# Performance work log

Measured on AMD Instinct MI355X. Metric: run time of the kernel, lower is better.

The kernel has to match this reference:

```python
import jax, jax.numpy as jnp
import numpy as np
from jax import lax

N = 512  # neurons (== input features in this base class)

@jax.custom_vjp
def spike_fn(x):
    # Heaviside spike with fast-sigmoid surrogate gradient (standard for LIF SNNs)
    return (x > 0.0).astype(x.dtype)

def _spike_fwd(x):
    return spike_fn(x), x

def _spike_bwd(x, g):
    sg = 1.0 / (1.0 + 10.0 * jnp.abs(x)) ** 2
    return (g * sg,)

spike_fn.defvjp(_spike_fwd, _spike_bwd)

def setup_inputs() -> dict:
    key = jax.random.key(0)
    k1, k2, k3, k4, k5, k6 = jax.random.split(key, 6)
    B, T = 64, 1000
    scale = 1.0 / np.sqrt(N)
    return {
        "input_batch": jax.random.normal(k1, (B, T, N), dtype=jnp.float32),
        "state_snn": jnp.zeros((2, B, N), dtype=jnp.float32),  # [v; s]
        "state_LI": jnp.zeros((B, N), dtype=jnp.float32),
        "W1": jax.random.normal(k2, (N, N), dtype=jnp.float32) * scale,
        "W2": jax.random.normal(k3, (N, N), dtype=jnp.float32) * scale,
        "leak_v": jax.random.uniform(k4, (N,), dtype=jnp.float32, minval=0.8, maxval=0.99),
        "leak_i": jax.random.uniform(k5, (N,), dtype=jnp.float32, minval=0.8, maxval=0.99),
        "thresh": jax.random.uniform(k6, (N,), dtype=jnp.float32, minval=0.5, maxval=1.5),
    }

def reference(input_batch, state_snn, state_LI, W1, W2, leak_v, leak_i, thresh):
    # input_batch: [B, T, N]; time loop expressed as lax.scan over T
    v0, s0 = state_snn[0], state_snn[1]
    xs = jnp.swapaxes(input_batch, 0, 1)  # [T, B, N]

    def step(carry, x_t):
        v, s, u = carry
        ff = x_t @ W1.T                        # LIF feed-forward current
        v = leak_v * v * (1.0 - s) + ff        # leak + reset-to-zero on spike
        s = spike_fn(v - thresh)               # spike generation
        u = leak_i * u + s @ W2.T              # leaky-integrator readout
        return (v, s, u), (s, jnp.stack([v, s]), u)

    _, (spikes, states_snn, decoded) = lax.scan(step, (v0, s0, state_LI), xs)
    # spikes: [T,B,N], states_snn: [T,2,B,N], decoded: [T,B,N]
    return spikes, states_snn, decoded
```

## Files before the change

kernel.cpp:

```cpp
#include <hip/hip_runtime.h>

#define T_STEPS 1000
#define B_SZ 64
#define N_SZ 512
#define BN_TOT (B_SZ * N_SZ)
#define TBN   ((size_t)T_STEPS * BN_TOT)

typedef __attribute__((ext_vector_type(4))) float f32x4;
typedef __attribute__((ext_vector_type(8))) short bf16x8;
typedef unsigned short ushort_t;

__global__ __launch_bounds__(256, 2)
void sgemm_abt(const float* __restrict__ A, const float* __restrict__ W,
               float* __restrict__ C)
{
    constexpr int K = 512;
    constexpr int BK = 32;
    constexpr int LDT = 128 + 4;
    __shared__ float As[BK][LDT];
    __shared__ float Bs[BK][LDT];

    const int tid = threadIdx.x;
    const int tx = tid & 15;
    const int ty = tid >> 4;
    const size_t m0 = (size_t)blockIdx.y * 128;
    const int n0 = blockIdx.x * 128;

    float acc[8][8];
#pragma unroll
    for (int i = 0; i < 8; ++i)
#pragma unroll
        for (int j = 0; j < 8; ++j) acc[i][j] = 0.0f;

    for (int k0 = 0; k0 < K; k0 += BK) {
#pragma unroll
        for (int p = 0; p < 4; ++p) {
            int i = tid + p * 256;
            int r = i >> 3;
            int q = i & 7;
            float4 va = *(const float4*)(A + (m0 + r) * K + k0 + q * 4);
            As[q * 4 + 0][r] = va.x; As[q * 4 + 1][r] = va.y;
            As[q * 4 + 2][r] = va.z; As[q * 4 + 3][r] = va.w;
            float4 vb = *(const float4*)(W + (size_t)(n0 + r) * K + k0 + q * 4);
            Bs[q * 4 + 0][r] = vb.x; Bs[q * 4 + 1][r] = vb.y;
            Bs[q * 4 + 2][r] = vb.z; Bs[q * 4 + 3][r] = vb.w;
        }
        __syncthreads();
#pragma unroll
        for (int k = 0; k < BK; ++k) {
            float a[8], b[8];
            *(float4*)&a[0] = *(const float4*)&As[k][ty * 8];
            *(float4*)&a[4] = *(const float4*)&As[k][ty * 8 + 4];
            *(float4*)&b[0] = *(const float4*)&Bs[k][tx * 4];
            *(float4*)&b[4] = *(const float4*)&Bs[k][tx * 4 + 64];
#pragma unroll
            for (int i = 0; i < 8; ++i)
#pragma unroll
                for (int j = 0; j < 8; ++j)
                    acc[i][j] = fmaf(a[i], b[j], acc[i][j]);
        }
        __syncthreads();
    }

#pragma unroll
    for (int i = 0; i < 8; ++i) {
        float* cp = C + (m0 + ty * 8 + i) * 512 + n0 + tx * 4;
        *(float4*)cp        = make_float4(acc[i][0], acc[i][1], acc[i][2], acc[i][3]);
        *(float4*)(cp + 64) = make_float4(acc[i][4], acc[i][5], acc[i][6], acc[i][7]);
    }
}

__global__ __launch_bounds__(256)
void w2_split(const float* __restrict__ W2, ushort_t* __restrict__ Wc)
{
    int i = blockIdx.x * 256 + threadIdx.x;
    int n = i >> 9, k = i & 511;
    float w = W2[i];
    unsigned wb = __float_as_uint(w);
    float h = __uint_as_float(wb & 0xFFFF0000u);
    float r1 = w - h;
    unsigned r1b = __float_as_uint(r1);
    size_t base = (size_t)n * 1024 + k;
    Wc[base]       = (ushort_t)(wb >> 16);
    Wc[base + 512] = (ushort_t)(r1b >> 16);
}

__global__ __launch_bounds__(256, 2)
void gemm2_mfma(const ushort_t* __restrict__ S, const ushort_t* __restrict__ Wc,
                float* __restrict__ C)
{
    constexpr int NT = 1024 / 32;
    __shared__ ushort_t As[2][128 * 32];
    __shared__ ushort_t Bs[2][128 * 32];

    const int tid = threadIdx.x;
    const int m0 = blockIdx.y * 128;
    const int n0 = blockIdx.x * 128;
    const int wid = tid >> 6;
    const int lane = tid & 63;
    const int wm = (wid >> 1) * 64;
    const int wn = (wid & 1) * 64;
    const int fr = lane & 15;
    const int fq = lane >> 4;

    f32x4 acc[4][4] = {};

    const int rA = tid >> 2;
    const int cA = (tid & 3) * 8;

#define STAGE(buf, t)                                                        \
    {                                                                        \
        const int k0_ = (t) * 32;                                            \
        const int kk_ = k0_ & 511;         \
        _Pragma("unroll")                                                    \
        for (int i = 0; i < 2; ++i) {                                        \
            __builtin_amdgcn_global_load_lds(                                \
                (const __attribute__((address_space(1))) unsigned int*)      \
                    (S + (size_t)(m0 + i * 64 + rA) * 512 + kk_ + cA),       \
                (__attribute__((address_space(3))) unsigned int*)            \
                    (As[buf] + i * 2048 + tid * 8),                          \
                16, 0, 0);                                                   \
            __builtin_amdgcn_global_load_lds(                                \
                (const __attribute__((address_space(1))) unsigned int*)      \
                    (Wc + (size_t)(n0 + i * 64 + rA) * 1024 + k0_ + cA),     \
                (__attribute__((address_space(3))) unsigned int*)            \
                    (Bs[buf] + i * 2048 + tid * 8),                          \
                16, 0, 0);                                                   \
        }                                                                    \
    }

    STAGE(0, 0);
    asm volatile("s_waitcnt vmcnt(0)" ::: "memory");
    __syncthreads();

    int cur = 0;
    for (int t = 0; t < NT; ++t) {
        if (t + 1 < NT)
            STAGE(cur ^ 1, t + 1);

        bf16x8 a[4], b[4];
#pragma unroll
        for (int m = 0; m < 4; ++m)
            a[m] = *(const bf16x8*)(As[cur] + (wm + m * 16 + fr) * 32 + fq * 8);
#pragma unroll
        for (int n = 0; n < 4; ++n)
            b[n] = *(const bf16x8*)(Bs[cur] + (wn + n * 16 + fr) * 32 + fq * 8);
#pragma unroll
        for (int m = 0; m < 4; ++m)
#pragma unroll
            for (int n = 0; n < 4; ++n)
                acc[m][n] = __builtin_amdgcn_mfma_f32_16x16x32_bf16(
                    a[m], b[n], acc[m][n], 0, 0, 0);

        asm volatile("s_waitcnt vmcnt(0)" ::: "memory");
        __syncthreads();
        cur ^= 1;
    }
#undef STAGE

#pragma unroll
    for (int m = 0; m < 4; ++m) {
        const int row = m0 + wm + m * 16 + fq * 4;
#pragma unroll
        for (int n = 0; n < 4; ++n) {
            const int col = n0 + wn + n * 16 + fr;
#pragma unroll
            for (int j = 0; j < 4; ++j)
                C[(size_t)(row + j) * 512 + col] = acc[m][n][j];
        }
    }
}

__global__ __launch_bounds__(128)
void lif_scan(const float* __restrict__ ff, const float* __restrict__ st0,
              const float* __restrict__ leak_v, const float* __restrict__ thresh,
              float* __restrict__ spikes, float* __restrict__ states,
              ushort_t* __restrict__ sbf)
{
    const int idx = blockIdx.x * 128 + threadIdx.x;
    const int n = idx & (N_SZ - 1);
    const int b = idx >> 9;

    float v = st0[idx];
    float s = st0[BN_TOT + idx];
    const float lv = leak_v[n];
    const float th = thresh[n];

    const float* fp = ff + (size_t)b * T_STEPS * N_SZ + n;
    float* sp  = spikes + idx;
    float* stp = states + idx;
    ushort_t* sbp = sbf ? (sbf + idx) : (ushort_t*)0;

    float f0 = fp[0], f1 = fp[N_SZ], f2 = fp[2 * N_SZ], f3 = fp[3 * N_SZ];

    for (int t = 0; t < T_STEPS; t += 4) {
        float g0 = 0.f, g1 = 0.f, g2 = 0.f, g3 = 0.f;
        if (t + 4 < T_STEPS) {
            const float* q = fp + (size_t)(t + 4) * N_SZ;
            g0 = q[0]; g1 = q[N_SZ]; g2 = q[2 * N_SZ]; g3 = q[3 * N_SZ];
        }
#define LIF_STEP(F, TOFF)                                                  \
        {                                                                  \
            v = lv * v * (1.0f - s) + (F);                                 \
            s = (v > th) ? 1.0f : 0.0f;                                    \
            size_t o  = (size_t)(t + (TOFF)) * BN_TOT;                     \
            size_t o2 = (size_t)(t + (TOFF)) * (2 * BN_TOT);               \
            sp[o] = s;                                                     \
            stp[o2] = v;                                                   \
            stp[o2 + BN_TOT] = s;                                          \
            if (sbp) sbp[o] = (ushort_t)(__float_as_uint(s) >> 16);        \
        }
        LIF_STEP(f0, 0) LIF_STEP(f1, 1) LIF_STEP(f2, 2) LIF_STEP(f3, 3)
#undef LIF_STEP
        f0 = g0; f1 = g1; f2 = g2; f3 = g3;
    }
}

__global__ __launch_bounds__(128)
void li_scan(float* __restrict__ dec, const float* __restrict__ u0,
             const float* __restrict__ leak_i)
{
    const int idx = blockIdx.x * 128 + threadIdx.x;
    const int n = idx & (N_SZ - 1);

    float u = u0[idx];
    const float li = leak_i[n];
    float* p = dec + idx;

    float y0 = p[0], y1 = p[BN_TOT], y2 = p[2 * (size_t)BN_TOT], y3 = p[3 * (size_t)BN_TOT];

    for (int t = 0; t < T_STEPS; t += 4) {
        float g0 = 0.f, g1 = 0.f, g2 = 0.f, g3 = 0.f;
        if (t + 4 < T_STEPS) {
            float* q = p + (size_t)(t + 4) * BN_TOT;
            g0 = q[0]; g1 = q[BN_TOT]; g2 = q[2 * (size_t)BN_TOT]; g3 = q[3 * (size_t)BN_TOT];
        }
#define LI_STEP(Y, TOFF)                                                   \
        {                                                                  \
            u = fmaf(li, u, (Y));                                          \
            p[(size_t)(t + (TOFF)) * BN_TOT] = u;                          \
        }
        LI_STEP(y0, 0) LI_STEP(y1, 1) LI_STEP(y2, 2) LI_STEP(y3, 3)
#undef LI_STEP
        y0 = g0; y1 = g1; y2 = g2; y3 = g3;
    }
}

extern "C" void kernel_launch(void* const* d_in, const int* in_sizes, int n_in,
                              void* d_out, int out_size, void* d_ws, size_t ws_size,
                              hipStream_t stream)
{
    (void)in_sizes; (void)n_in; (void)out_size;

    const float* X     = (const float*)d_in[0];
    const float* st_sn = (const float*)d_in[1];
    const float* st_li = (const float*)d_in[2];
    const float* W1    = (const float*)d_in[3];
    const float* W2    = (const float*)d_in[4];
    const float* lv    = (const float*)d_in[5];
    const float* li    = (const float*)d_in[6];
    const float* th    = (const float*)d_in[7];

    float* spikes = (float*)d_out;
    float* states = spikes + TBN;
    float* dec    = states + 2 * TBN;

    const size_t WS_NEED = (size_t)512 * 1024 * 2 + (size_t)64000 * 512 * 2;
    const bool use_mfma = (ws_size >= WS_NEED);
    ushort_t* Wc = (ushort_t*)d_ws;
    ushort_t* Sb = Wc + (size_t)512 * 1024;

    const dim3 gemm_grid(4, 500), gemm_block(256);
    const dim3 scan_grid(BN_TOT / 128), scan_block(128);

    if (use_mfma)
        w2_split<<<dim3(1024), dim3(256), 0, stream>>>(W2, Wc);

    sgemm_abt<<<gemm_grid, gemm_block, 0, stream>>>(X, W1, dec);

    lif_scan<<<scan_grid, scan_block, 0, stream>>>(dec, st_sn, lv, th,
                                                   spikes, states,
                                                   use_mfma ? Sb : (ushort_t*)0);

    if (use_mfma)
        gemm2_mfma<<<gemm_grid, gemm_block, 0, stream>>>(Sb, Wc, dec);
    else
        sgemm_abt<<<gemm_grid, gemm_block, 0, stream>>>(spikes, W2, dec);

    li_scan<<<scan_grid, scan_block, 0, stream>>>(dec, st_li, li);
}
```

Baseline: 798.3 us.

## Double-buffer shared tiles and XOR-swizzle LDS layout in feed-forward SGEMM

After: 1.038 ms. 1.3x slower.

```diff
diff --git a/kernel.cpp b/kernel.cpp
--- a/kernel.cpp
+++ b/kernel.cpp
@@ -16,9 +16,10 @@
 {
     constexpr int K = 512;
     constexpr int BK = 32;
+    constexpr int NT = K / BK;
     constexpr int LDT = 128 + 4;
-    __shared__ float As[BK][LDT];
-    __shared__ float Bs[BK][LDT];
+    __shared__ float As[2][BK][LDT];
+    __shared__ float Bs[2][BK][LDT];
 
     const int tid = threadIdx.x;
     const int tx = tid & 15;
@@ -32,35 +33,51 @@
 #pragma unroll
         for (int j = 0; j < 8; ++j) acc[i][j] = 0.0f;
 
-    for (int k0 = 0; k0 < K; k0 += BK) {
-#pragma unroll
-        for (int p = 0; p < 4; ++p) {
-            int i = tid + p * 256;
-            int r = i >> 3;
-            int q = i & 7;
-            float4 va = *(const float4*)(A + (m0 + r) * K + k0 + q * 4);
-            As[q * 4 + 0][r] = va.x; As[q * 4 + 1][r] = va.y;
-            As[q * 4 + 2][r] = va.z; As[q * 4 + 3][r] = va.w;
-            float4 vb = *(const float4*)(W + (size_t)(n0 + r) * K + k0 + q * 4);
-            Bs[q * 4 + 0][r] = vb.x; Bs[q * 4 + 1][r] = vb.y;
-            Bs[q * 4 + 2][r] = vb.z; Bs[q * 4 + 3][r] = vb.w;
-        }
-        __syncthreads();
+#define STAGE(buf, kt)                                                       \
+    {                                                                        \
+        const int k0_ = (kt) * BK;                                           \
+        _Pragma("unroll")                                                    \
+        for (int p = 0; p < 4; ++p) {                                        \
+            int i = tid + p * 256;                                           \
+            int r = i >> 3;                             \
+            int q = i & 7;                              \
+            int rs = r ^ (q << 3);                      \
+            float4 va = *(const float4*)(A + (m0 + r) * K + k0_ + q * 4);    \
+            As[buf][q * 4 + 0][rs] = va.x; As[buf][q * 4 + 1][rs] = va.y;    \
+            As[buf][q * 4 + 2][rs] = va.z; As[buf][q * 4 + 3][rs] = va.w;    \
+            float4 vb = *(const float4*)(W + (size_t)(n0 + r) * K + k0_ + q * 4); \
+            Bs[buf][q * 4 + 0][rs] = vb.x; Bs[buf][q * 4 + 1][rs] = vb.y;    \
+            Bs[buf][q * 4 + 2][rs] = vb.z; Bs[buf][q * 4 + 3][rs] = vb.w;    \
+        }                                                                    \
+    }
+
+    STAGE(0, 0);
+    __syncthreads();
+
+    int cur = 0;
+    for (int kt = 0; kt < NT; ++kt) {
+        if (kt + 1 < NT)
+            STAGE(cur ^ 1, kt + 1);
+
 #pragma unroll
         for (int k = 0; k < BK; ++k) {
+            const int s8 = (k >> 2) << 3;
             float a[8], b[8];
-            *(float4*)&a[0] = *(const float4*)&As[k][ty * 8];
-            *(float4*)&a[4] = *(const float4*)&As[k][ty * 8 + 4];
-            *(float4*)&b[0] = *(const float4*)&Bs[k][tx * 4];
-            *(float4*)&b[4] = *(const float4*)&Bs[k][tx * 4 + 64];
+            *(float4*)&a[0] = *(const float4*)&As[cur][k][(ty * 8) ^ s8];
+            *(float4*)&a[4] = *(const float4*)&As[cur][k][((ty * 8) ^ s8) + 4];
+            *(float4*)&b[0] = *(const float4*)&Bs[cur][k][(tx * 4) ^ s8];
+            *(float4*)&b[4] = *(const float4*)&Bs[cur][k][((tx * 4) ^ s8) + 64];
 #pragma unroll
             for (int i = 0; i < 8; ++i)
 #pragma unroll
                 for (int j = 0; j < 8; ++j)
                     acc[i][j] = fmaf(a[i], b[j], acc[i][j]);
         }
+
         __syncthreads();
-    }
+        cur ^= 1;
+    }
+#undef STAGE
 
 #pragma unroll
     for (int i = 0; i < 8; ++i) {
```
